# Performance work log

Measured on AMD Instinct MI355X. Metric: run time of the kernel, lower is better.

## Reference

```python
import jax, jax.numpy as jnp
import numpy as np

ROPE_BASE = 10000.0

def _rope_cos_sin(seq_len, head_dim, dtype):
    half = head_dim // 2
    inv_freq = 1.0 / (ROPE_BASE ** (jnp.arange(0, half, dtype=jnp.float32) / half))
    ang = jnp.arange(seq_len, dtype=jnp.float32)[:, None] * inv_freq[None, :]  # [S, half]
    ang = jnp.concatenate([ang, ang], axis=-1)  # [S, D]
    return jnp.cos(ang).astype(dtype), jnp.sin(ang).astype(dtype)

def _rotate_half(t):
    d = t.shape[-1] // 2
    return jnp.concatenate([-t[..., d:], t[..., :d]], axis=-1)

def _apply_rope(t, cos, sin):
    # t: [B, H, S, D]; cos/sin: [S, D]
    return t * cos[None, None, :, :] + _rotate_half(t) * sin[None, None, :, :]

def setup_inputs() -> dict:
    key = jax.random.key(0)
    ks = jax.random.split(key, 6)
    B, S, DM = 2, 2048, 2048
    x = jax.random.normal(ks[0], (B, S, DM), dtype=jnp.float32)
    attention_mask = jnp.ones((B, S), dtype=jnp.bool_)
    scale = 1.0 / np.sqrt(DM)
    W_in = jax.random.normal(ks[1], (DM, 3 * DM), dtype=jnp.float32) * scale
    b_in = jax.random.normal(ks[2], (3 * DM,), dtype=jnp.float32) * 0.02
    W_out = jax.random.normal(ks[3], (DM, DM), dtype=jnp.float32) * scale
    b_out = jax.random.normal(ks[4], (DM,), dtype=jnp.float32) * 0.02
    return {"x": x, "attention_mask": attention_mask, "W_in": W_in,
            "b_in": b_in, "W_out": W_out, "b_out": b_out}

def reference(x, attention_mask, W_in, b_in, W_out, b_out):
    B, S, DM = x.shape
    H = 16
    D = DM // H
    qkv = x @ W_in + b_in                         # [B, S, 3*DM]
    q, k, v = jnp.split(qkv, 3, axis=-1)
    def to_heads(t):
        return t.reshape(B, S, H, D).transpose(0, 2, 1, 3)  # [B, H, S, D]
    q, k, v = to_heads(q), to_heads(k), to_heads(v)
    cos, sin = _rope_cos_sin(S, D, x.dtype)
    q = _apply_rope(q, cos, sin)
    k = _apply_rope(k, cos, sin)
    scale = 1.0 / np.sqrt(D).astype(np.float32)
    scores = jnp.einsum('bhqd,bhkd->bhqk', q, k) * scale   # [B, H, S, S]
    # SDPA bool mask semantics: True = attend, False = mask out
    mask = attention_mask[:, None, None, :]
    scores = jnp.where(mask, scores, jnp.finfo(scores.dtype).min)
    attn = jax.nn.softmax(scores, axis=-1)
    out = jnp.einsum('bhqk,bhkd->bhqd', attn, v)           # [B, H, S, D]
    out = out.transpose(0, 2, 1, 3).reshape(B, S, DM)
    return out @ W_out + b_out
```

## Files before the change

### kernel.cpp

```cpp
#include <hip/hip_runtime.h>
#include <math.h>

typedef _Float16 f16;
typedef _Float16 f16x4 __attribute__((ext_vector_type(4)));
typedef _Float16 f16x8 __attribute__((ext_vector_type(8)));
typedef float    f32x4 __attribute__((ext_vector_type(4)));

__device__ __forceinline__ void lds_async16(void* lds, const void* g) {
  __builtin_amdgcn_global_load_lds(
      (const __attribute__((address_space(1))) void*)g,
      (__attribute__((address_space(3))) void*)lds, 16, 0, 0);
}

__device__ __forceinline__ f16x4 shfl8(f16x4 v, int srcLane) {
  union { f16x4 h; int i[2]; } u;
  u.h = v;
  u.i[0] = __shfl(u.i[0], srcLane, 64);
  u.i[1] = __shfl(u.i[1], srcLane, 64);
  return u.h;
}

#define BARRIER_FENCE() do { __builtin_amdgcn_s_barrier(); asm volatile("" ::: "memory"); } while (0)
#define WAIT_LGKM0()    asm volatile("s_waitcnt lgkmcnt(0)" ::: "memory")


__global__ __launch_bounds__(256) void f2h4_kernel(const float* __restrict__ in,
                                                   f16* __restrict__ out, int n4) {
  int i = blockIdx.x * 256 + threadIdx.x;
  if (i < n4) {
    float4 v = ((const float4*)in)[i];
    f16x4 h;
    h.x = (f16)v.x; h.y = (f16)v.y; h.z = (f16)v.z; h.w = (f16)v.w;
    ((f16x4*)out)[i] = h;
  }
}

__global__ __launch_bounds__(256) void transpose_f2h(const float* __restrict__ in,
                                                     f16* __restrict__ out,
                                                     int rows, int cols) {
  __shared__ f16 t[64][65];
  int r0 = blockIdx.x * 64, c0 = blockIdx.y * 64;
  int tid = threadIdx.x;
#pragma unroll
  for (int i = 0; i < 16; ++i) {
    int idx = i * 256 + tid;
    int r = idx >> 6, c = idx & 63;
    t[r][c] = (f16)in[(size_t)(r0 + r) * cols + c0 + c];
  }
  __syncthreads();
#pragma unroll
  for (int i = 0; i < 16; ++i) {
    int idx = i * 256 + tid;
    int c = idx >> 6, r = idx & 63;
    out[(size_t)(c0 + c) * rows + r0 + r] = t[r][c];
  }
}

__global__ __launch_bounds__(256) void rope_table_k(float* __restrict__ cosT,
                                                    float* __restrict__ sinT) {
  int idx = blockIdx.x * 256 + threadIdx.x;
  int s = idx >> 6, j = idx & 63;
  double invf = pow(10000.0, -(double)j / 64.0);
  double a = fmod((double)s * invf, 6.283185307179586476925287);
  cosT[s * 64 + j] = (float)cos(a);
  sinT[s * 64 + j] = (float)sin(a);
}

__global__ __launch_bounds__(256, 2) void gemm_qkv(const f16* __restrict__ A,
                                                   const f16* __restrict__ Bt,
                                                   const float* __restrict__ bias,
                                                   const float* __restrict__ cosT,
                                                   const float* __restrict__ sinT,
                                                   f16* __restrict__ Qh, f16* __restrict__ Kh,
                                                   f16* __restrict__ Vt) {
  const int Kd = 2048;
  __shared__ __align__(16) f16 smem[32768];
  f16* Asb = smem;
  f16* Bsb = smem + 16384;
  int tid = threadIdx.x;
  int lane = tid & 63, wave = tid >> 6;
  int wm = wave >> 1, wn = wave & 1;
  int l15 = lane & 15, l4 = lane >> 4;
  int bn = blockIdx.x * 128, bm = blockIdx.y * 128;

  auto stageAq = [&](int buf, int kt, int qh) {
#pragma unroll
    for (int i = 0; i < 2; ++i) {
      int c = i * 256 + tid;
      int rl = c >> 3, gl = c & 7;
      int row = qh * 32 + (rl & 31) + (rl >> 5) * 64;
      int gg = gl ^ (rl & 7);
      lds_async16(&Asb[buf * 8192 + row * 64 + gl * 8],
                  A + (size_t)(bm + row) * Kd + kt * 64 + gg * 8);
    }
  };
  auto stageBh = [&](int buf, int kt, int h) {
#pragma unroll
    for (int i = 0; i < 2; ++i) {
      int c = i * 256 + tid;
      int rl = c >> 3, gl = c & 7;
      int row = h * 64 + rl;
      int gg = gl ^ (rl & 7);
      lds_async16(&Bsb[buf * 8192 + row * 64 + gl * 8],
                  Bt + (size_t)(bn + row) * Kd + kt * 64 + gg * 8);
    }
  };

  f32x4 acc[4][4] = {};

  stageAq(0, 0, 0); stageAq(0, 0, 1); stageBh(0, 0, 0); stageBh(0, 0, 1);
  stageAq(1, 1, 0); stageBh(1, 1, 0);
  asm volatile("s_waitcnt vmcnt(4)" ::: "memory");
  BARRIER_FENCE();

  for (int t = 0; t < 32; ++t) {
    int cb = t & 1;
    const f16* as = Asb + cb * 8192;
    const f16* bs = Bsb + cb * 8192;
    f16x8 af[2], bf[4];

#pragma unroll
    for (int j = 0; j < 2; ++j)
      af[j] = *(const f16x8*)&as[(wm * 64 + j * 16 + l15) * 64 + ((l4 ^ (l15 & 7)) * 8)];
#pragma unroll
    for (int nf = 0; nf < 4; ++nf) {
      int gr = (nf & 1) * 4 + (nf >> 1) + wn * 2;
      bf[nf] = *(const f16x8*)&bs[(gr * 16 + l15) * 64 + ((l4 ^ (l15 & 7)) * 8)];
    }
    if (t + 1 < 32) { stageAq(cb ^ 1, t + 1, 1); stageBh(cb ^ 1, t + 1, 1); }
    BARRIER_FENCE();
    WAIT_LGKM0();
    __builtin_amdgcn_s_setprio(1);
#pragma unroll
    for (int j = 0; j < 2; ++j)
#pragma unroll
      for (int nf = 0; nf < 4; ++nf)
        acc[j][nf] = __builtin_amdgcn_mfma_f32_16x16x32_f16(af[j], bf[nf], acc[j][nf], 0, 0, 0);
    __builtin_amdgcn_s_setprio(0);
    BARRIER_FENCE();

#pragma unroll
    for (int j = 0; j < 2; ++j)
      af[j] = *(const f16x8*)&as[(wm * 64 + (2 + j) * 16 + l15) * 64 + ((l4 ^ (l15 & 7)) * 8)];
    BARRIER_FENCE();
    WAIT_LGKM0();
    __builtin_amdgcn_s_setprio(1);
#pragma unroll
    for (int j = 0; j < 2; ++j)
#pragma unroll
      for (int nf = 0; nf < 4; ++nf)
        acc[2 + j][nf] = __builtin_amdgcn_mfma_f32_16x16x32_f16(af[j], bf[nf], acc[2 + j][nf], 0, 0, 0);
    __builtin_amdgcn_s_setprio(0);
    BARRIER_FENCE();

#pragma unroll
    for (int j = 0; j < 2; ++j)
      af[j] = *(const f16x8*)&as[(wm * 64 + j * 16 + l15) * 64 + (((4 + l4) ^ (l15 & 7)) * 8)];
#pragma unroll
    for (int nf = 0; nf < 4; ++nf) {
      int gr = (nf & 1) * 4 + (nf >> 1) + wn * 2;
      bf[nf] = *(const f16x8*)&bs[(gr * 16 + l15) * 64 + (((4 + l4) ^ (l15 & 7)) * 8)];
    }
    BARRIER_FENCE();
    WAIT_LGKM0();
    __builtin_amdgcn_s_setprio(1);
#pragma unroll
    for (int j = 0; j < 2; ++j)
#pragma unroll
      for (int nf = 0; nf < 4; ++nf)
        acc[j][nf] = __builtin_amdgcn_mfma_f32_16x16x32_f16(af[j], bf[nf], acc[j][nf], 0, 0, 0);
    __builtin_amdgcn_s_setprio(0);
    BARRIER_FENCE();

#pragma unroll
    for (int j = 0; j < 2; ++j)
      af[j] = *(const f16x8*)&as[(wm * 64 + (2 + j) * 16 + l15) * 64 + (((4 + l4) ^ (l15 & 7)) * 8)];
    if (t + 2 < 32) { stageAq(cb, t + 2, 0); stageBh(cb, t + 2, 0); }
    BARRIER_FENCE();
    WAIT_LGKM0();
    __builtin_amdgcn_s_setprio(1);
#pragma unroll
    for (int j = 0; j < 2; ++j)
#pragma unroll
      for (int nf = 0; nf < 4; ++nf)
        acc[2 + j][nf] = __builtin_amdgcn_mfma_f32_16x16x32_f16(af[j], bf[nf], acc[2 + j][nf], 0, 0, 0);
    __builtin_amdgcn_s_setprio(0);
    if (t < 30) asm volatile("s_waitcnt vmcnt(4)" ::: "memory");
    else        asm volatile("s_waitcnt vmcnt(0)" ::: "memory");
    BARRIER_FENCE();
  }

  int which = bn >> 11;
  int head  = (bn & 2047) >> 7;
  if (which < 2) {
    f16* dst = which == 0 ? Qh : Kh;
    const float qsc = which == 0 ? 0.08838834764831845f : 1.0f;
#pragma unroll
    for (int mi = 0; mi < 4; ++mi)
#pragma unroll
      for (int r = 0; r < 4; ++r) {
        int gm = bm + wm * 64 + mi * 16 + l4 * 4 + r;
        int b = gm >> 11, s = gm & 2047;
        size_t rowbase = ((size_t)(b * 16 + head) * 2048 + s) << 7;
#pragma unroll
        for (int p = 0; p < 2; ++p) {
          int dlo = (p + wn * 2) * 16 + l15;
          float cth = cosT[s * 64 + dlo], sth = sinT[s * 64 + dlo];
          float lo = acc[mi][2 * p][r]     + bias[bn + dlo];
          float hi = acc[mi][2 * p + 1][r] + bias[bn + dlo + 64];
          dst[rowbase + dlo]      = (f16)((lo * cth - hi * sth) * qsc);
          dst[rowbase + dlo + 64] = (f16)((hi * cth + lo * sth) * qsc);
        }
      }
  } else {
    __syncthreads();
    f16* Vsc = smem;
#pragma unroll
    for (int mi = 0; mi < 4; ++mi)
#pragma unroll
      for (int nf = 0; nf < 4; ++nf) {
        int d = ((nf & 1) * 4 + (nf >> 1) + wn * 2) * 16 + l15;
        int s = wm * 64 + mi * 16 + l4 * 4;
        f16x4 v;
#pragma unroll
        for (int r = 0; r < 4; ++r) v[r] = (f16)(acc[mi][nf][r] + bias[bn + d]);
        int off = d * 128 + ((((s >> 3) ^ ((d & 7) << 1))) << 3) + (s & 7);
        *(f16x4*)&Vsc[off] = v;
      }
    __syncthreads();
    int bm2 = bm & 2047, b = bm >> 11;
#pragma unroll
    for (int it = 0; it < 8; ++it) {
      int idx = it * 256 + tid;
      int d = idx >> 4, gs = idx & 15;
      f16x8 v = *(const f16x8*)&Vsc[d * 128 + ((gs ^ ((d & 7) << 1)) << 3)];
      *(f16x8*)&Vt[((size_t)(b * 16 + head) * 128 + d) * 2048 + bm2 + gs * 8] = v;
    }
  }
}

__global__ __launch_bounds__(256, 2) void gemm_out(const f16* __restrict__ A,
                                                   const f16* __restrict__ Bt,
                                                   const float* __restrict__ bias,
                                                   float* __restrict__ C) {
  const int Kd = 2048, Nd = 2048;
  __shared__ __align__(16) f16 smem[32768];
  f16* Asb = smem;
  f16* Bsb = smem + 16384;
  int tid = threadIdx.x;
  int lane = tid & 63, wave = tid >> 6;
  int wm = wave >> 1, wn = wave & 1;
  int l15 = lane & 15, l4 = lane >> 4;
  int bm = blockIdx.x * 128, bn = blockIdx.y * 128;

  auto stageAq = [&](int buf, int kt, int qh) {
#pragma unroll
    for (int i = 0; i < 2; ++i) {
      int c = i * 256 + tid;
      int rl = c >> 3, gl = c & 7;
      int row = qh * 32 + (rl & 31) + (rl >> 5) * 64;
      int gg = gl ^ (rl & 7);
      lds_async16(&Asb[buf * 8192 + row * 64 + gl * 8],
                  A + (size_t)(bm + row) * Kd + kt * 64 + gg * 8);
    }
  };
  auto stageBh = [&](int buf, int kt, int h) {
#pragma unroll
    for (int i = 0; i < 2; ++i) {
      int c = i * 256 + tid;
      int rl = c >> 3, gl = c & 7;
      int row = h * 64 + rl;
      int gg = gl ^ (rl & 7);
      lds_async16(&Bsb[buf * 8192 + row * 64 + gl * 8],
                  Bt + (size_t)(bn + row) * Kd + kt * 64 + gg * 8);
    }
  };

  f32x4 acc[4][4] = {};

  stageAq(0, 0, 0); stageAq(0, 0, 1); stageBh(0, 0, 0); stageBh(0, 0, 1);
  stageAq(1, 1, 0); stageBh(1, 1, 0);
  asm volatile("s_waitcnt vmcnt(4)" ::: "memory");
  BARRIER_FENCE();

  for (int t = 0; t < 32; ++t) {
    int cb = t & 1;
    const f16* as = Asb + cb * 8192;
    const f16* bs = Bsb + cb * 8192;
    f16x8 af[2], bf[4];

#pragma unroll
    for (int j = 0; j < 2; ++j)
      af[j] = *(const f16x8*)&as[(wm * 64 + j * 16 + l15) * 64 + ((l4 ^ (l15 & 7)) * 8)];
#pragma unroll
    for (int nf = 0; nf < 4; ++nf)
      bf[nf] = *(const f16x8*)&bs[(wn * 64 + nf * 16 + l15) * 64 + ((l4 ^ (l15 & 7)) * 8)];
    if (t + 1 < 32) { stageAq(cb ^ 1, t + 1, 1); stageBh(cb ^ 1, t + 1, 1); }
    BARRIER_FENCE();
    WAIT_LGKM0();
    __builtin_amdgcn_s_setprio(1);
#pragma unroll
    for (int j = 0; j < 2; ++j)
#pragma unroll
      for (int nf = 0; nf < 4; ++nf)
        acc[j][nf] = __builtin_amdgcn_mfma_f32_16x16x32_f16(af[j], bf[nf], acc[j][nf], 0, 0, 0);
    __builtin_amdgcn_s_setprio(0);
    BARRIER_FENCE();

#pragma unroll
    for (int j = 0; j < 2; ++j)
      af[j] = *(const f16x8*)&as[(wm * 64 + (2 + j) * 16 + l15) * 64 + ((l4 ^ (l15 & 7)) * 8)];
    BARRIER_FENCE();
    WAIT_LGKM0();
    __builtin_amdgcn_s_setprio(1);
#pragma unroll
    for (int j = 0; j < 2; ++j)
#pragma unroll
      for (int nf = 0; nf < 4; ++nf)
        acc[2 + j][nf] = __builtin_amdgcn_mfma_f32_16x16x32_f16(af[j], bf[nf], acc[2 + j][nf], 0, 0, 0);
    __builtin_amdgcn_s_setprio(0);
    BARRIER_FENCE();

#pragma unroll
    for (int j = 0; j < 2; ++j)
      af[j] = *(const f16x8*)&as[(wm * 64 + j * 16 + l15) * 64 + (((4 + l4) ^ (l15 & 7)) * 8)];
#pragma unroll
    for (int nf = 0; nf < 4; ++nf)
      bf[nf] = *(const f16x8*)&bs[(wn * 64 + nf * 16 + l15) * 64 + (((4 + l4) ^ (l15 & 7)) * 8)];
    BARRIER_FENCE();
    WAIT_LGKM0();
    __builtin_amdgcn_s_setprio(1);
#pragma unroll
    for (int j = 0; j < 2; ++j)
#pragma unroll
      for (int nf = 0; nf < 4; ++nf)
        acc[j][nf] = __builtin_amdgcn_mfma_f32_16x16x32_f16(af[j], bf[nf], acc[j][nf], 0, 0, 0);
    __builtin_amdgcn_s_setprio(0);
    BARRIER_FENCE();

#pragma unroll
    for (int j = 0; j < 2; ++j)
      af[j] = *(const f16x8*)&as[(wm * 64 + (2 + j) * 16 + l15) * 64 + (((4 + l4) ^ (l15 & 7)) * 8)];
    if (t + 2 < 32) { stageAq(cb, t + 2, 0); stageBh(cb, t + 2, 0); }
    BARRIER_FENCE();
    WAIT_LGKM0();
    __builtin_amdgcn_s_setprio(1);
#pragma unroll
    for (int j = 0; j < 2; ++j)
#pragma unroll
      for (int nf = 0; nf < 4; ++nf)
        acc[2 + j][nf] = __builtin_amdgcn_mfma_f32_16x16x32_f16(af[j], bf[nf], acc[2 + j][nf], 0, 0, 0);
    __builtin_amdgcn_s_setprio(0);
    if (t < 30) asm volatile("s_waitcnt vmcnt(4)" ::: "memory");
    else        asm volatile("s_waitcnt vmcnt(0)" ::: "memory");
    BARRIER_FENCE();
  }

#pragma unroll
  for (int mi = 0; mi < 4; ++mi)
#pragma unroll
    for (int nf = 0; nf < 4; ++nf)
#pragma unroll
      for (int r = 0; r < 4; ++r) {
        int gm = bm + wm * 64 + mi * 16 + l4 * 4 + r;
        int gn = bn + wn * 64 + nf * 16 + l15;
        C[(size_t)gm * Nd + gn] = acc[mi][nf][r] + bias[gn];
      }
}

__global__ __launch_bounds__(256, 2) void attn_fwd(const f16* __restrict__ Qh,
                                                   const f16* __restrict__ Kh,
                                                   const f16* __restrict__ Vt,
                                                   f16* __restrict__ O) {
  __shared__ f16 Ks[2][64 * 128];
  __shared__ f16 Vs[2][128 * 64];
  int tid = threadIdx.x, lane = tid & 63, wave = tid >> 6;
  int l15 = lane & 15, l4 = lane >> 4;
  int qt = blockIdx.x, bh = blockIdx.y;
  size_t head = (size_t)bh * (2048 * 128);

  f16x8 qf[2][4];
#pragma unroll
  for (int g = 0; g < 2; ++g) {
    const f16* qrow = Qh + head + (size_t)(qt * 128 + wave * 32 + g * 16 + l15) * 128;
#pragma unroll
    for (int ks = 0; ks < 4; ++ks) qf[g][ks] = *(const f16x8*)(qrow + ks * 32 + l4 * 8);
  }

  auto stage = [&](int buf, int kt) {
#pragma unroll
    for (int i = 0; i < 4; ++i) {
      int c = i * 256 + tid;
      int r = c >> 4, gl = c & 15, gg = gl ^ (r & 15);
      lds_async16(&Ks[buf][c * 8], Kh + head + (size_t)(kt * 64 + r) * 128 + gg * 8);
    }
#pragma unroll
    for (int i = 0; i < 4; ++i) {
      int c = i * 256 + tid;
      int r = c >> 3, gl = c & 7, gg = gl ^ (r & 7);
      lds_async16(&Vs[buf][c * 8], Vt + head + (size_t)r * 2048 + kt * 64 + gg * 8);
    }
  };

  f32x4 acc_o[2][8] = {};
  float m_i[2] = {-1e30f, -1e30f}, l_i[2] = {0.f, 0.f};
  int srcLo = 32 * (l4 & 1) + l15;
  int sel = l4 >> 1;

  stage(0, 0);
  for (int kt = 0; kt < 32; ++kt) {
    int cur = kt & 1;
    __syncthreads();
    if (kt < 31) stage(cur ^ 1, kt + 1);

    f32x4 accs[2][4] = {};
#pragma unroll
    for (int ks = 0; ks < 4; ++ks) {
#pragma unroll
      for (int ms = 0; ms < 4; ++ms) {
        int row = ms * 16 + l15;
        int gl = (ks * 4 + l4) ^ l15;
        f16x8 a = *(const f16x8*)&Ks[cur][row * 128 + gl * 8];
        accs[0][ms] = __builtin_amdgcn_mfma_f32_16x16x32_f16(a, qf[0][ks], accs[0][ms], 0, 0, 0);
        accs[1][ms] = __builtin_amdgcn_mfma_f32_16x16x32_f16(a, qf[1][ks], accs[1][ms], 0, 0, 0);
      }
    }
    f16x8 afrag[2][2];
#pragma unroll
    for (int g = 0; g < 2; ++g) {
      float mx = -1e30f;
#pragma unroll
      for (int ms = 0; ms < 4; ++ms)
#pragma unroll
        for (int r = 0; r < 4; ++r) mx = fmaxf(mx, accs[g][ms][r]);
      mx = fmaxf(mx, __shfl_xor(mx, 16));
      mx = fmaxf(mx, __shfl_xor(mx, 32));
      bool skip = __all(mx - m_i[g] <= 8.0f);
      float mnew, alpha;
      if (skip) {
        mnew = m_i[g];
      } else {
        mnew = fmaxf(m_i[g], mx);
        alpha = __expf(m_i[g] - mnew);
        m_i[g] = mnew;
      }
      float rsum = 0.f;
      f16x4 pv4[4];
#pragma unroll
      for (int ms = 0; ms < 4; ++ms) {
#pragma unroll
        for (int r = 0; r < 4; ++r) {
          float p = __expf(accs[g][ms][r] - mnew);
          rsum += p;
          pv4[ms][r] = (f16)p;
        }
      }
      rsum += __shfl_xor(rsum, 16);
      rsum += __shfl_xor(rsum, 32);
      if (skip) {
        l_i[g] += rsum;
      } else {
        float al[4];
#pragma unroll
        for (int r = 0; r < 4; ++r) al[r] = __shfl(alpha, l4 * 4 + r);
#pragma unroll
        for (int ns = 0; ns < 8; ++ns)
#pragma unroll
          for (int r = 0; r < 4; ++r) acc_o[g][ns][r] *= al[r];
        l_i[g] = l_i[g] * alpha + rsum;
      }
#pragma unroll
      for (int ks = 0; ks < 2; ++ks) {
        f16x4 a0 = shfl8(pv4[2 * ks],     srcLo);
        f16x4 b0 = shfl8(pv4[2 * ks + 1], srcLo);
        f16x4 a1 = shfl8(pv4[2 * ks],     srcLo + 16);
        f16x4 b1 = shfl8(pv4[2 * ks + 1], srcLo + 16);
        f16x4 lo, hi;
        if (sel) { lo = b0; hi = b1; } else { lo = a0; hi = a1; }
        afrag[g][ks][0] = lo[0]; afrag[g][ks][1] = lo[1]; afrag[g][ks][2] = lo[2]; afrag[g][ks][3] = lo[3];
        afrag[g][ks][4] = hi[0]; afrag[g][ks][5] = hi[1]; afrag[g][ks][6] = hi[2]; afrag[g][ks][7] = hi[3];
      }
    }
#pragma unroll
    for (int ks = 0; ks < 2; ++ks) {
#pragma unroll
      for (int ns = 0; ns < 8; ++ns) {
        int row = ns * 16 + l15;
        int gl = (ks * 4 + l4) ^ (l15 & 7);
        f16x8 b = *(const f16x8*)&Vs[cur][row * 64 + gl * 8];
        acc_o[0][ns] = __builtin_amdgcn_mfma_f32_16x16x32_f16(afrag[0][ks], b, acc_o[0][ns], 0, 0, 0);
        acc_o[1][ns] = __builtin_amdgcn_mfma_f32_16x16x32_f16(afrag[1][ks], b, acc_o[1][ns], 0, 0, 0);
      }
    }
  }
  int b = bh >> 4, h = bh & 15;
#pragma unroll
  for (int g = 0; g < 2; ++g) {
    float inv[4];
#pragma unroll
    for (int r = 0; r < 4; ++r) inv[r] = 1.0f / __shfl(l_i[g], l4 * 4 + r);
#pragma unroll
    for (int ns = 0; ns < 8; ++ns)
#pragma unroll
      for (int r = 0; r < 4; ++r) {
        int q = qt * 128 + wave * 32 + g * 16 + l4 * 4 + r;
        int col = h * 128 + ns * 16 + l15;
        O[((size_t)(b * 2048 + q)) * 2048 + col] = (f16)(acc_o[g][ns][r] * inv[r]);
      }
  }
}


extern "C" void kernel_launch(void* const* d_in, const int* in_sizes, int n_in,
                              void* d_out, int out_size, void* d_ws, size_t ws_size,
                              hipStream_t stream) {
  const float* x     = (const float*)d_in[0];
  const float* W_in  = (const float*)d_in[2];
  const float* b_in  = (const float*)d_in[3];
  const float* W_out = (const float*)d_in[4];
  const float* b_out = (const float*)d_in[5];
  float* out = (float*)d_out;

  char* w = (char*)d_ws;
  f16*   Xh    = (f16*)(w);
  f16*   WinT  = (f16*)(w + 16777216ull);
  f16*   WoutT = (f16*)(w + 41943040ull);
  float* cosT  = (float*)(w + 50331648ull);
  float* sinT  = (float*)(w + 51380224ull);
  f16*   Qh    = (f16*)(w + 52428800ull);
  f16*   Kh    = (f16*)(w + 69206016ull);
  f16*   A2    = (f16*)(w + 85983232ull);
  f16*   Vt    = (f16*)(w + 102760448ull);

  f2h4_kernel<<<dim3(8192), dim3(256), 0, stream>>>(x, Xh, 8388608 / 4);
  transpose_f2h<<<dim3(32, 96), dim3(256), 0, stream>>>(W_in, WinT, 2048, 6144);
  transpose_f2h<<<dim3(32, 32), dim3(256), 0, stream>>>(W_out, WoutT, 2048, 2048);
  rope_table_k<<<dim3(512), dim3(256), 0, stream>>>(cosT, sinT);
  gemm_qkv<<<dim3(48, 32), dim3(256), 0, stream>>>(Xh, WinT, b_in, cosT, sinT, Qh, Kh, Vt);
  attn_fwd<<<dim3(16, 32), dim3(256), 0, stream>>>(Qh, Kh, Vt, A2);
  gemm_out<<<dim3(32, 16), dim3(256), 0, stream>>>(A2, WoutT, b_out, out);
}
```

Measured before the change: 386.5 us.

## Use 8-wave 512-thread blocks in both GEMMs with smaller per-wave tiles

Result: slower. 395.8 us (+2.4%).

```diff
diff --git a/kernel.cpp b/kernel.cpp
--- a/kernel.cpp
+++ b/kernel.cpp
@@ -66,7 +66,7 @@
   sinT[s * 64 + j] = (float)sin(a);
 }
 
-__global__ __launch_bounds__(256, 2) void gemm_qkv(const f16* __restrict__ A,
+__global__ __launch_bounds__(512, 4) void gemm_qkv(const f16* __restrict__ A,
                                                    const f16* __restrict__ Bt,
                                                    const float* __restrict__ bias,
                                                    const float* __restrict__ cosT,
@@ -79,54 +79,44 @@
   f16* Bsb = smem + 16384;
   int tid = threadIdx.x;
   int lane = tid & 63, wave = tid >> 6;
-  int wm = wave >> 1, wn = wave & 1;
+  int wm = wave >> 2, wn = wave & 3;
   int l15 = lane & 15, l4 = lane >> 4;
   int bn = blockIdx.x * 128, bm = blockIdx.y * 128;
 
   auto stageAq = [&](int buf, int kt, int qh) {
-#pragma unroll
-    for (int i = 0; i < 2; ++i) {
-      int c = i * 256 + tid;
-      int rl = c >> 3, gl = c & 7;
-      int row = qh * 32 + (rl & 31) + (rl >> 5) * 64;
-      int gg = gl ^ (rl & 7);
-      lds_async16(&Asb[buf * 8192 + row * 64 + gl * 8],
-                  A + (size_t)(bm + row) * Kd + kt * 64 + gg * 8);
-    }
+    int rl = tid >> 3, gl = tid & 7;
+    int row = qh * 32 + (rl & 31) + (rl >> 5) * 64;
+    int gg = gl ^ (rl & 7);
+    lds_async16(&Asb[buf * 8192 + row * 64 + gl * 8],
+                A + (size_t)(bm + row) * Kd + kt * 64 + gg * 8);
   };
   auto stageBh = [&](int buf, int kt, int h) {
-#pragma unroll
-    for (int i = 0; i < 2; ++i) {
-      int c = i * 256 + tid;
-      int rl = c >> 3, gl = c & 7;
-      int row = h * 64 + rl;
-      int gg = gl ^ (rl & 7);
-      lds_async16(&Bsb[buf * 8192 + row * 64 + gl * 8],
-                  Bt + (size_t)(bn + row) * Kd + kt * 64 + gg * 8);
-    }
+    int rl = tid >> 3, gl = tid & 7;
+    int row = h * 64 + rl;
+    int gg = gl ^ (rl & 7);
+    lds_async16(&Bsb[buf * 8192 + row * 64 + gl * 8],
+                Bt + (size_t)(bn + row) * Kd + kt * 64 + gg * 8);
   };
 
-  f32x4 acc[4][4] = {};
+  f32x4 acc[4][2] = {};
 
   stageAq(0, 0, 0); stageAq(0, 0, 1); stageBh(0, 0, 0); stageBh(0, 0, 1);
   stageAq(1, 1, 0); stageBh(1, 1, 0);
-  asm volatile("s_waitcnt vmcnt(4)" ::: "memory");
+  asm volatile("s_waitcnt vmcnt(2)" ::: "memory");
   BARRIER_FENCE();
 
   for (int t = 0; t < 32; ++t) {
     int cb = t & 1;
     const f16* as = Asb + cb * 8192;
     const f16* bs = Bsb + cb * 8192;
-    f16x8 af[2], bf[4];
+    f16x8 af[2], bf[2];
 
 #pragma unroll
     for (int j = 0; j < 2; ++j)
       af[j] = *(const f16x8*)&as[(wm * 64 + j * 16 + l15) * 64 + ((l4 ^ (l15 & 7)) * 8)];
 #pragma unroll
-    for (int nf = 0; nf < 4; ++nf) {
-      int gr = (nf & 1) * 4 + (nf >> 1) + wn * 2;
-      bf[nf] = *(const f16x8*)&bs[(gr * 16 + l15) * 64 + ((l4 ^ (l15 & 7)) * 8)];
-    }
+    for (int nf = 0; nf < 2; ++nf)
+      bf[nf] = *(const f16x8*)&bs[((wn + nf * 4) * 16 + l15) * 64 + ((l4 ^ (l15 & 7)) * 8)];
     if (t + 1 < 32) { stageAq(cb ^ 1, t + 1, 1); stageBh(cb ^ 1, t + 1, 1); }
     BARRIER_FENCE();
     WAIT_LGKM0();
@@ -134,7 +124,7 @@
 #pragma unroll
     for (int j = 0; j < 2; ++j)
 #pragma unroll
-      for (int nf = 0; nf < 4; ++nf)
+      for (int nf = 0; nf < 2; ++nf)
         acc[j][nf] = __builtin_amdgcn_mfma_f32_16x16x32_f16(af[j], bf[nf], acc[j][nf], 0, 0, 0);
     __builtin_amdgcn_s_setprio(0);
     BARRIER_FENCE();
@@ -148,7 +138,7 @@
 #pragma unroll
     for (int j = 0; j < 2; ++j)
 #pragma unroll
-      for (int nf = 0; nf < 4; ++nf)
+      for (int nf = 0; nf < 2; ++nf)
         acc[2 + j][nf] = __builtin_amdgcn_mfma_f32_16x16x32_f16(af[j], bf[nf], acc[2 + j][nf], 0, 0, 0);
     __builtin_amdgcn_s_setprio(0);
     BARRIER_FENCE();
@@ -157,17 +147,15 @@
     for (int j = 0; j < 2; ++j)
       af[j] = *(const f16x8*)&as[(wm * 64 + j * 16 + l15) * 64 + (((4 + l4) ^ (l15 & 7)) * 8)];
 #pragma unroll
-    for (int nf = 0; nf < 4; ++nf) {
-      int gr = (nf & 1) * 4 + (nf >> 1) + wn * 2;
-      bf[nf] = *(const f16x8*)&bs[(gr * 16 + l15) * 64 + (((4 + l4) ^ (l15 & 7)) * 8)];
-    }
-    BARRIER_FENCE();
-    WAIT_LGKM0();
-    __builtin_amdgcn_s_setprio(1);
-#pragma unroll
-    for (int j = 0; j < 2; ++j)
-#pragma unroll
-      for (int nf = 0; nf < 4; ++nf)
+    for (int nf = 0; nf < 2; ++nf)
+      bf[nf] = *(const f16x8*)&bs[((wn + nf * 4) * 16 + l15) * 64 + (((4 + l4) ^ (l15 & 7)) * 8)];
+    BARRIER_FENCE();
+    WAIT_LGKM0();
+    __builtin_amdgcn_s_setprio(1);
+#pragma unroll
+    for (int j = 0; j < 2; ++j)
+#pragma unroll
+      for (int nf = 0; nf < 2; ++nf)
         acc[j][nf] = __builtin_amdgcn_mfma_f32_16x16x32_f16(af[j], bf[nf], acc[j][nf], 0, 0, 0);
     __builtin_amdgcn_s_setprio(0);
     BARRIER_FENCE();
@@ -175,17 +163,17 @@
 #pragma unroll
     for (int j = 0; j < 2; ++j)
       af[j] = *(const f16x8*)&as[(wm * 64 + (2 + j) * 16 + l15) * 64 + (((4 + l4) ^ (l15 & 7)) * 8)];
-    if (t + 2 < 32) { stageAq(cb, t + 2, 0); stageBh(cb, t + 2, 0); }
-    BARRIER_FENCE();
-    WAIT_LGKM0();
-    __builtin_amdgcn_s_setprio(1);
-#pragma unroll
-    for (int j = 0; j < 2; ++j)
-#pragma unroll
-      for (int nf = 0; nf < 4; ++nf)
+    if (t + 2 < 32) { stageBh(cb, t + 2, 0); stageAq(cb, t + 2, 0); }
+    BARRIER_FENCE();
+    WAIT_LGKM0();
+    __builtin_amdgcn_s_setprio(1);
+#pragma unroll
+    for (int j = 0; j < 2; ++j)
+#pragma unroll
+      for (int nf = 0; nf < 2; ++nf)
         acc[2 + j][nf] = __builtin_amdgcn_mfma_f32_16x16x32_f16(af[j], bf[nf], acc[2 + j][nf], 0, 0, 0);
     __builtin_amdgcn_s_setprio(0);
-    if (t < 30) asm volatile("s_waitcnt vmcnt(4)" ::: "memory");
+    if (t < 30) asm volatile("s_waitcnt vmcnt(2)" ::: "memory");
     else        asm volatile("s_waitcnt vmcnt(0)" ::: "memory");
     BARRIER_FENCE();
   }
@@ -195,6 +183,7 @@
   if (which < 2) {
     f16* dst = which == 0 ? Qh : Kh;
     const float qsc = which == 0 ? 0.08838834764831845f : 1.0f;
+    int dlo = wn * 16 + l15;
 #pragma unroll
     for (int mi = 0; mi < 4; ++mi)
 #pragma unroll
@@ -202,15 +191,11 @@
         int gm = bm + wm * 64 + mi * 16 + l4 * 4 + r;
         int b = gm >> 11, s = gm & 2047;
         size_t rowbase = ((size_t)(b * 16 + head) * 2048 + s) << 7;
-#pragma unroll
-        for (int p = 0; p < 2; ++p) {
-          int dlo = (p + wn * 2) * 16 + l15;
-          float cth = cosT[s * 64 + dlo], sth = sinT[s * 64 + dlo];
-          float lo = acc[mi][2 * p][r]     + bias[bn + dlo];
-          float hi = acc[mi][2 * p + 1][r] + bias[bn + dlo + 64];
-          dst[rowbase + dlo]      = (f16)((lo * cth - hi * sth) * qsc);
-          dst[rowbase + dlo + 64] = (f16)((hi * cth + lo * sth) * qsc);
-        }
+        float cth = cosT[s * 64 + dlo], sth = sinT[s * 64 + dlo];
+        float lo = acc[mi][0][r] + bias[bn + dlo];
+        float hi = acc[mi][1][r] + bias[bn + dlo + 64];
+        dst[rowbase + dlo]      = (f16)((lo * cth - hi * sth) * qsc);
+        dst[rowbase + dlo + 64] = (f16)((hi * cth + lo * sth) * qsc);
       }
   } else {
     __syncthreads();
@@ -218,8 +203,8 @@
 #pragma unroll
     for (int mi = 0; mi < 4; ++mi)
 #pragma unroll
-      for (int nf = 0; nf < 4; ++nf) {
-        int d = ((nf & 1) * 4 + (nf >> 1) + wn * 2) * 16 + l15;
+      for (int nf = 0; nf < 2; ++nf) {
+        int d = (wn + nf * 4) * 16 + l15;
         int s = wm * 64 + mi * 16 + l4 * 4;
         f16x4 v;
 #pragma unroll
@@ -230,8 +215,8 @@
     __syncthreads();
     int bm2 = bm & 2047, b = bm >> 11;
 #pragma unroll
-    for (int it = 0; it < 8; ++it) {
-      int idx = it * 256 + tid;
+    for (int it = 0; it < 4; ++it) {
+      int idx = it * 512 + tid;
       int d = idx >> 4, gs = idx & 15;
       f16x8 v = *(const f16x8*)&Vsc[d * 128 + ((gs ^ ((d & 7) << 1)) << 3)];
       *(f16x8*)&Vt[((size_t)(b * 16 + head) * 128 + d) * 2048 + bm2 + gs * 8] = v;
@@ -239,7 +224,7 @@
   }
 }
 
-__global__ __launch_bounds__(256, 2) void gemm_out(const f16* __restrict__ A,
+__global__ __launch_bounds__(512, 4) void gemm_out(const f16* __restrict__ A,
                                                    const f16* __restrict__ Bt,
                                                    const float* __restrict__ bias,
                                                    float* __restrict__ C) {
@@ -249,52 +234,44 @@
   f16* Bsb = smem + 16384;
   int tid = threadIdx.x;
   int lane = tid & 63, wave = tid >> 6;
-  int wm = wave >> 1, wn = wave & 1;
+  int wm = wave >> 2, wn = wave & 3;
   int l15 = lane & 15, l4 = lane >> 4;
   int bm = blockIdx.x * 128, bn = blockIdx.y * 128;
 
   auto stageAq = [&](int buf, int kt, int qh) {
-#pragma unroll
-    for (int i = 0; i < 2; ++i) {
-      int c = i * 256 + tid;
-      int rl = c >> 3, gl = c & 7;
-      int row = qh * 32 + (rl & 31) + (rl >> 5) * 64;
-      int gg = gl ^ (rl & 7);
-      lds_async16(&Asb[buf * 8192 + row * 64 + gl * 8],
-                  A + (size_t)(bm + row) * Kd + kt * 64 + gg * 8);
-    }
+    int rl = tid >> 3, gl = tid & 7;
+    int row = qh * 32 + (rl & 31) + (rl >> 5) * 64;
+    int gg = gl ^ (rl & 7);
+    lds_async16(&Asb[buf * 8192 + row * 64 + gl * 8],
+                A + (size_t)(bm + row) * Kd + kt * 64 + gg * 8);
   };
   auto stageBh = [&](int buf, int kt, int h) {
-#pragma unroll
-    for (int i = 0; i < 2; ++i) {
-      int c = i * 256 + tid;
-      int rl = c >> 3, gl = c & 7;
-      int row = h * 64 + rl;
-      int gg = gl ^ (rl & 7);
-      lds_async16(&Bsb[buf * 8192 + row * 64 + gl * 8],
-                  Bt + (size_t)(bn + row) * Kd + kt * 64 + gg * 8);
-    }
+    int rl = tid >> 3, gl = tid & 7;
+    int row = h * 64 + rl;
+    int gg = gl ^ (rl & 7);
+    lds_async16(&Bsb[buf * 8192 + row * 64 + gl * 8],
+                Bt + (size_t)(bn + row) * Kd + kt * 64 + gg * 8);
   };
 
-  f32x4 acc[4][4] = {};
+  f32x4 acc[4][2] = {};
 
   stageAq(0, 0, 0); stageAq(0, 0, 1); stageBh(0, 0, 0); stageBh(0, 0, 1);
   stageAq(1, 1, 0); stageBh(1, 1, 0);
-  asm volatile("s_waitcnt vmcnt(4)" ::: "memory");
+  asm volatile("s_waitcnt vmcnt(2)" ::: "memory");
   BARRIER_FENCE();
 
   for (int t = 0; t < 32; ++t) {
     int cb = t & 1;
     const f16* as = Asb + cb * 8192;
     const f16* bs = Bsb + cb * 8192;
-    f16x8 af[2], bf[4];
+    f16x8 af[2], bf[2];
 
 #pragma unroll
     for (int j = 0; j < 2; ++j)
       af[j] = *(const f16x8*)&as[(wm * 64 + j * 16 + l15) * 64 + ((l4 ^ (l15 & 7)) * 8)];
 #pragma unroll
-    for (int nf = 0; nf < 4; ++nf)
-      bf[nf] = *(const f16x8*)&bs[(wn * 64 + nf * 16 + l15) * 64 + ((l4 ^ (l15 & 7)) * 8)];
+    for (int nf = 0; nf < 2; ++nf)
+      bf[nf] = *(const f16x8*)&bs[(wn * 32 + nf * 16 + l15) * 64 + ((l4 ^ (l15 & 7)) * 8)];
     if (t + 1 < 32) { stageAq(cb ^ 1, t + 1, 1); stageBh(cb ^ 1, t + 1, 1); }
     BARRIER_FENCE();
     WAIT_LGKM0();
@@ -302,7 +279,7 @@
 #pragma unroll
     for (int j = 0; j < 2; ++j)
 #pragma unroll
-      for (int nf = 0; nf < 4; ++nf)
+      for (int nf = 0; nf < 2; ++nf)
         acc[j][nf] = __builtin_amdgcn_mfma_f32_16x16x32_f16(af[j], bf[nf], acc[j][nf], 0, 0, 0);
     __builtin_amdgcn_s_setprio(0);
     BARRIER_FENCE();
@@ -316,7 +293,7 @@
 #pragma unroll
     for (int j = 0; j < 2; ++j)
 #pragma unroll
-      for (int nf = 0; nf < 4; ++nf)
+      for (int nf = 0; nf < 2; ++nf)
         acc[2 + j][nf] = __builtin_amdgcn_mfma_f32_16x16x32_f16(af[j], bf[nf], acc[2 + j][nf], 0, 0, 0);
     __builtin_amdgcn_s_setprio(0);
     BARRIER_FENCE();
@@ -325,15 +302,15 @@
     for (int j = 0; j < 2; ++j)
       af[j] = *(const f16x8*)&as[(wm * 64 + j * 16 + l15) * 64 + (((4 + l4) ^ (l15 & 7)) * 8)];
 #pragma unroll
-    for (int nf = 0; nf < 4; ++nf)
-      bf[nf] = *(const f16x8*)&bs[(wn * 64 + nf * 16 + l15) * 64 + (((4 + l4) ^ (l15 & 7)) * 8)];
-    BARRIER_FENCE();
-    WAIT_LGKM0();
-    __builtin_amdgcn_s_setprio(1);
-#pragma unroll
-    for (int j = 0; j < 2; ++j)
-#pragma unroll
-      for (int nf = 0; nf < 4; ++nf)
+    for (int nf = 0; nf < 2; ++nf)
+      bf[nf] = *(const f16x8*)&bs[(wn * 32 + nf * 16 + l15) * 64 + (((4 + l4) ^ (l15 & 7)) * 8)];
+    BARRIER_FENCE();
+    WAIT_LGKM0();
+    __builtin_amdgcn_s_setprio(1);
+#pragma unroll
+    for (int j = 0; j < 2; ++j)
+#pragma unroll
+      for (int nf = 0; nf < 2; ++nf)
         acc[j][nf] = __builtin_amdgcn_mfma_f32_16x16x32_f16(af[j], bf[nf], acc[j][nf], 0, 0, 0);
     __builtin_amdgcn_s_setprio(0);
     BARRIER_FENCE();
@@ -341,17 +318,17 @@
 #pragma unroll
     for (int j = 0; j < 2; ++j)
       af[j] = *(const f16x8*)&as[(wm * 64 + (2 + j) * 16 + l15) * 64 + (((4 + l4) ^ (l15 & 7)) * 8)];
-    if (t + 2 < 32) { stageAq(cb, t + 2, 0); stageBh(cb, t + 2, 0); }
-    BARRIER_FENCE();
-    WAIT_LGKM0();
-    __builtin_amdgcn_s_setprio(1);
-#pragma unroll
-    for (int j = 0; j < 2; ++j)
-#pragma unroll
-      for (int nf = 0; nf < 4; ++nf)
+    if (t + 2 < 32) { stageBh(cb, t + 2, 0); stageAq(cb, t + 2, 0); }
+    BARRIER_FENCE();
+    WAIT_LGKM0();
+    __builtin_amdgcn_s_setprio(1);
+#pragma unroll
+    for (int j = 0; j < 2; ++j)
+#pragma unroll
+      for (int nf = 0; nf < 2; ++nf)
         acc[2 + j][nf] = __builtin_amdgcn_mfma_f32_16x16x32_f16(af[j], bf[nf], acc[2 + j][nf], 0, 0, 0);
     __builtin_amdgcn_s_setprio(0);
-    if (t < 30) asm volatile("s_waitcnt vmcnt(4)" ::: "memory");
+    if (t < 30) asm volatile("s_waitcnt vmcnt(2)" ::: "memory");
     else        asm volatile("s_waitcnt vmcnt(0)" ::: "memory");
     BARRIER_FENCE();
   }
@@ -359,11 +336,11 @@
 #pragma unroll
   for (int mi = 0; mi < 4; ++mi)
 #pragma unroll
-    for (int nf = 0; nf < 4; ++nf)
+    for (int nf = 0; nf < 2; ++nf)
 #pragma unroll
       for (int r = 0; r < 4; ++r) {
         int gm = bm + wm * 64 + mi * 16 + l4 * 4 + r;
-        int gn = bn + wn * 64 + nf * 16 + l15;
+        int gn = bn + wn * 32 + nf * 16 + l15;
         C[(size_t)gm * Nd + gn] = acc[mi][nf][r] + bias[gn];
       }
 }
@@ -536,7 +513,7 @@
   transpose_f2h<<<dim3(32, 96), dim3(256), 0, stream>>>(W_in, WinT, 2048, 6144);
   transpose_f2h<<<dim3(32, 32), dim3(256), 0, stream>>>(W_out, WoutT, 2048, 2048);
   rope_table_k<<<dim3(512), dim3(256), 0, stream>>>(cosT, sinT);
-  gemm_qkv<<<dim3(48, 32), dim3(256), 0, stream>>>(Xh, WinT, b_in, cosT, sinT, Qh, Kh, Vt);
+  gemm_qkv<<<dim3(48, 32), dim3(512), 0, stream>>>(Xh, WinT, b_in, cosT, sinT, Qh, Kh, Vt);
   attn_fwd<<<dim3(16, 32), dim3(256), 0, stream>>>(Qh, Kh, Vt, A2);
-  gemm_out<<<dim3(32, 16), dim3(256), 0, stream>>>(A2, WoutT, b_out, out);
-}
+  gemm_out<<<dim3(32, 16), dim3(512), 0, stream>>>(A2, WoutT, b_out, out);
+}
```
